# Performance work log

Hardware: AMD Instinct MI355X
Metric: run time of the kernel (lower is better)

## Reference

```python
import jax, jax.numpy as jnp
import numpy as np

H = 768      # hidden_size
NH = 12      # num_attention_heads
DH = H // NH # attention_head_size
FF = 3072    # intermediate_size
E = 4        # n_expert
B, S = 8, 512
EPS = 1e-12


def _layernorm(x, g, b):
    mu = jnp.mean(x, axis=-1, keepdims=True)
    var = jnp.var(x, axis=-1, keepdims=True)
    return (x - mu) * jax.lax.rsqrt(var + EPS) * g + b


def _expert_linear(x, W, b, expert_idx):
    # W: [E, in, out], b: [E, out]; gather per-sample expert weights, then batched GEMM.
    # Mathematically identical to running every expert then slicing (single_select_fwd).
    Wg = W[expert_idx]            # [B, in, out]
    bg = b[expert_idx]            # [B, out]
    return jnp.einsum('bsi,bio->bso', x, Wg) + bg[:, None, :]


def setup_inputs() -> dict:
    key = jax.random.key(0)
    ks = jax.random.split(key, 16)
    sc = 0.02
    inp = {
        'hidden_states': jax.random.normal(ks[0], (B, S, H), jnp.float32),
        'expert_idx': jax.random.randint(ks[1], (B,), 0, E, jnp.int64) if jax.config.read('jax_enable_x64') else jax.random.randint(ks[1], (B,), 0, E).astype(jnp.int32),
        'attention_mask': jnp.zeros((B, 1, 1, S), jnp.float32),
        'Wq': sc * jax.random.normal(ks[2], (E, H, H), jnp.float32),
        'bq': jnp.zeros((E, H), jnp.float32),
        'Wk': sc * jax.random.normal(ks[3], (E, H, H), jnp.float32),
        'bk': jnp.zeros((E, H), jnp.float32),
        'Wv': sc * jax.random.normal(ks[4], (E, H, H), jnp.float32),
        'bv': jnp.zeros((E, H), jnp.float32),
        'Wo': sc * jax.random.normal(ks[5], (E, H, H), jnp.float32),
        'bo': jnp.zeros((E, H), jnp.float32),
        'ln1_g': jnp.ones((H,), jnp.float32),
        'ln1_b': jnp.zeros((H,), jnp.float32),
        'Wi': sc * jax.random.normal(ks[6], (E, H, FF), jnp.float32),
        'bi': jnp.zeros((E, FF), jnp.float32),
        'Wout': sc * jax.random.normal(ks[7], (E, FF, H), jnp.float32),
        'bout': jnp.zeros((E, H), jnp.float32),
        'ln2_g': jnp.ones((H,), jnp.float32),
        'ln2_b': jnp.zeros((H,), jnp.float32),
    }
    return inp


def reference(hidden_states, expert_idx, attention_mask, Wq, bq, Wk, bk, Wv, bv,
              Wo, bo, ln1_g, ln1_b, Wi, bi, Wout, bout, ln2_g, ln2_b):
    b, s, h = hidden_states.shape
    # --- MoE self-attention (per-sample expert QKV) ---
    q = _expert_linear(hidden_states, Wq, bq, expert_idx).reshape(b, s, NH, DH).transpose(0, 2, 1, 3)
    k = _expert_linear(hidden_states, Wk, bk, expert_idx).reshape(b, s, NH, DH).transpose(0, 2, 1, 3)
    v = _expert_linear(hidden_states, Wv, bv, expert_idx).reshape(b, s, NH, DH).transpose(0, 2, 1, 3)
    scores = jnp.einsum('bhqd,bhkd->bhqk', q, k) / np.sqrt(DH).astype(np.float32)
    scores = scores + attention_mask
    probs = jax.nn.softmax(scores, axis=-1)
    ctx = jnp.einsum('bhqk,bhkd->bhqd', probs, v).transpose(0, 2, 1, 3).reshape(b, s, h)
    # --- MoE self-output: dense + residual + LN ---
    attn_out = _expert_linear(ctx, Wo, bo, expert_idx)
    x = _layernorm(attn_out + hidden_states, ln1_g, ln1_b)
    # --- MoE FFN: intermediate (GELU) + output + residual + LN ---
    hmid = jax.nn.gelu(_expert_linear(x, Wi, bi, expert_idx), approximate=False)
    ffn = _expert_linear(hmid, Wout, bout, expert_idx)
    return _layernorm(ffn + x, ln2_g, ln2_b)
```

## Files before the change

### kernel.cpp

```cpp
#include <hip/hip_runtime.h>
#include <cstdint>
#include <cstddef>

constexpr int CB  = 8;
constexpr int CS  = 512;
constexpr int CH  = 768;
constexpr int CNH = 12;
constexpr int CDH = 64;
constexpr int CFF = 3072;
constexpr int CE  = 4;
constexpr int C3H = 3 * CH;

using f32x4  = __attribute__((ext_vector_type(4))) float;
using bf16x8 = __attribute__((ext_vector_type(8))) short;

__device__ __forceinline__ short f2bf(float x) {
  union { float f; uint32_t u; } v; v.f = x;
  return (short)((v.u + 0x7fffu + ((v.u >> 16) & 1u)) >> 16);
}

__device__ __forceinline__ void gload_lds16(const void* g, void* l) {
  __builtin_amdgcn_global_load_lds((const __attribute__((address_space(1))) void*)g,
                                   (__attribute__((address_space(3))) void*)l,
                                   16, 0, 0);
}

#define VMCNT(n)  asm volatile("s_waitcnt vmcnt(" #n ")" ::: "memory")
#define SCHEDB()  __builtin_amdgcn_sched_barrier(0)

__global__ void cvt_bf16_kernel(const float* __restrict__ in, short* __restrict__ out, int n4) {
  int i = blockIdx.x * blockDim.x + threadIdx.x;
  if (i < n4) {
    float4 v = ((const float4*)in)[i];
    short4 o;
    o.x = f2bf(v.x); o.y = f2bf(v.y); o.z = f2bf(v.z); o.w = f2bf(v.w);
    ((short4*)out)[i] = o;
  }
}

__device__ __forceinline__ bool expert_used(const int* __restrict__ eidx, int e) {
  bool u = false;
#pragma unroll
  for (int s = 0; s < CB; ++s) u |= (eidx[s] == e);
  return u;
}

__device__ __forceinline__ void tpose_body(const float* __restrict__ Wb,
                                           short* __restrict__ Wtb, int K, int N) {
  __shared__ __align__(16) short Ts[64 * 68];
  const int n0 = blockIdx.x * 64, k0 = blockIdx.y * 64;
  const int t  = threadIdx.x;
  const int tn = t & 15, tk = t >> 4;
#pragma unroll
  for (int p = 0; p < 4; ++p) {
    int k = k0 + p * 16 + tk;
    float4 v = *(const float4*)(Wb + (size_t)k * N + n0 + tn * 4);
#pragma unroll
    for (int j = 0; j < 4; ++j)
      Ts[(tn * 4 + j) * 68 + p * 16 + tk] = f2bf(((const float*)&v)[j]);
  }
  __syncthreads();
#pragma unroll
  for (int p = 0; p < 4; ++p) {
    int n = n0 + p * 16 + tk;
    uint2 o = *(const uint2*)(Ts + (p * 16 + tk) * 68 + tn * 4);
    *(uint2*)(Wtb + (size_t)n * K + k0 + tn * 4) = o;
  }
}

__global__ void tpose_cvt_kernel(const float* __restrict__ W, short* __restrict__ Wt,
                                 const int* __restrict__ eidx, int K, int N) {
  const int e = blockIdx.z;
  if (!expert_used(eidx, e)) return;
  tpose_body(W + (size_t)e * K * N, Wt + (size_t)e * K * N, K, N);
}

__global__ void tpose4_kernel(const float* __restrict__ Wq, const float* __restrict__ Wk,
                              const float* __restrict__ Wv, const float* __restrict__ Wo,
                              const int* __restrict__ eidx,
                              short* __restrict__ Wqkvt, short* __restrict__ Wot) {
  const int z = blockIdx.z, e = z >> 2, m = z & 3;
  if (!expert_used(eidx, e)) return;
  const float* W = (m == 0) ? Wq : (m == 1) ? Wk : (m == 2) ? Wv : Wo;
  const float* Wb = W + (size_t)e * CH * CH;
  short* dst = (m == 3) ? (Wot + (size_t)e * CH * CH)
                        : (Wqkvt + ((size_t)e * C3H + m * CH) * CH);
  tpose_body(Wb, dst, CH, CH);
}

__global__ void qkv_bias_kernel(const float* __restrict__ bq, const float* __restrict__ bk,
                                const float* __restrict__ bv, float* __restrict__ dst) {
  int i = blockIdx.x * 256 + threadIdx.x;
  if (i >= CE * C3H) return;
  int e = i / C3H, r = i % C3H;
  int m = r / CH, c = r % CH;
  const float* s = (m == 0) ? bq : (m == 1) ? bk : bv;
  dst[i] = s[e * CH + c];
}

__device__ __forceinline__ void expert_sort(const int* __restrict__ eidx,
                                            uint32_t& epack, uint32_t& sortedPack) {
  int exv[CB];
#pragma unroll
  for (int s = 0; s < CB; ++s) exv[s] = eidx[s];
  epack = 0;
#pragma unroll
  for (int s = 0; s < CB; ++s) epack |= (uint32_t)exv[s] << (2 * s);
  int c0 = 0, c1 = 0, c2 = 0;
#pragma unroll
  for (int s = 0; s < CB; ++s) {
    c0 += (exv[s] == 0); c1 += (exv[s] == 1); c2 += (exv[s] == 2);
  }
  int p0 = 0, p1 = c0, p2 = c0 + c1, p3 = c0 + c1 + c2;
  sortedPack = 0;
#pragma unroll
  for (int s = 0; s < CB; ++s) {
    int ee = exv[s];
    int p = (ee == 0) ? p0 : (ee == 1) ? p1 : (ee == 2) ? p2 : p3;
    sortedPack |= (uint32_t)s << (4 * p);
    p0 += (ee == 0); p1 += (ee == 1); p2 += (ee == 2); p3 += (ee == 3);
  }
}

template <int BM, int NTN, int KSPLIT, int NJB, int NNB>
__device__ __forceinline__ void moe_decode(const int* __restrict__ eidx,
                                           int& e, int& mrow0, int& nt, int& ks) {
  constexpr int JC  = 4096 / BM;
  constexpr int MTS = CS / BM;
  constexpr int CHJ = JC / NJB;
  constexpr int CHN = NTN / NNB;
  constexpr int NKB = 8 / (NJB * NNB);
  constexpr int CHK = KSPLIT / NKB;
  uint32_t epack, sortedPack;
  expert_sort(eidx, epack, sortedPack);
  const int x = (int)blockIdx.x & 7;
  const int i = (int)blockIdx.x >> 3;
  const int kb = x / (NJB * NNB);
  const int rx = x - kb * (NJB * NNB);
  const int jb = rx / NNB, nb = rx - (rx / NNB) * NNB;
  const int nn = i % CHN;
  const int rem = i / CHN;
  const int jj = rem % CHJ;
  const int kk2 = rem / CHJ;
  const int j = jb * CHJ + jj;
  nt = nb * CHN + nn;
  ks = kb * CHK + kk2;
  const int sample = (int)((sortedPack >> (4 * (j / MTS))) & 7);
  e = (int)((epack >> (2 * sample)) & 3);
  mrow0 = sample * CS + (j % MTS) * BM;
}

template <int K, int NTN, int KSPLIT, int NJB, int NNB, int ACT, bool OB16>
__global__ __launch_bounds__(256, 2)
void gemm8_kernel(const short* __restrict__ A, const short* __restrict__ Wt,
                  const float* __restrict__ bias, const int* __restrict__ eidx,
                  char* __restrict__ out, char* __restrict__ out2,
                  size_t wtExpStride, int biasStride, int outLd, size_t outKsStride) {
  constexpr int BM = 128, BN = 192;
  constexpr int MI = 4, NI = 6;
  constexpr int NT = K / KSPLIT / 128;
  __shared__ __align__(16) short As[BM * 128];
  __shared__ __align__(16) short Bs[BN * 128];
  const int t = threadIdx.x, w = t >> 6, l = t & 63, lr = l & 15, lg = l >> 4;

  int e, mrow0, nt, ks;
  moe_decode<BM, NTN, KSPLIT, NJB, NNB>(eidx, e, mrow0, nt, ks);
  const int kBase = ks * NT * 128;

  const int srow = t >> 4;
  const int gcol = ((t & 15) ^ srow) * 8;
  const short* aSrc = A + (size_t)(mrow0 + srow) * K + kBase + gcol;
  const short* bSrc = Wt + (size_t)e * wtExpStride + (size_t)(nt * BN + srow) * K + kBase + gcol;
  const size_t iss16 = (size_t)16 * K;

  const int wrow = (w >> 1) * 64, wn = (w & 1) * 96;
  int aoff[4][MI], boff[4][NI];
#pragma unroll
  for (int kk = 0; kk < 4; ++kk) {
    const int c = (kk * 4 + lg) ^ lr;
#pragma unroll
    for (int mi = 0; mi < MI; ++mi)
      aoff[kk][mi] = (wrow + mi * 16 + lr) * 128 + c * 8;
#pragma unroll
    for (int ni = 0; ni < NI; ++ni)
      boff[kk][ni] = (wn + ni * 16 + lr) * 128 + c * 8;
  }

  f32x4 acc[MI][NI] = {};

  for (int kt = 0; kt < NT; ++kt) {
    {
      const short* as = aSrc + (size_t)kt * 128;
#pragma unroll
      for (int i = 0; i < 8; ++i)
        gload_lds16(as + i * iss16, &As[i * 2048 + t * 8]);
      const short* bs = bSrc + (size_t)kt * 128;
#pragma unroll
      for (int i = 0; i < 12; ++i)
        gload_lds16(bs + i * iss16, &Bs[i * 2048 + t * 8]);
    }
    VMCNT(0);
    __builtin_amdgcn_s_barrier();
    SCHEDB();
#pragma unroll
    for (int kk = 0; kk < 4; ++kk) {
      bf16x8 af[MI], bfr[NI];
#pragma unroll
      for (int ni = 0; ni < NI; ++ni) bfr[ni] = *(const bf16x8*)(&Bs[boff[kk][ni]]);
#pragma unroll
      for (int mi = 0; mi < MI; ++mi) af[mi] = *(const bf16x8*)(&As[aoff[kk][mi]]);
      __builtin_amdgcn_s_setprio(1);
#pragma unroll
      for (int mi = 0; mi < MI; ++mi)
#pragma unroll
        for (int ni = 0; ni < NI; ++ni)
          acc[mi][ni] = __builtin_amdgcn_mfma_f32_16x16x32_bf16(af[mi], bfr[ni],
                                                                acc[mi][ni], 0, 0, 0);
      __builtin_amdgcn_s_setprio(0);
    }
    __builtin_amdgcn_s_barrier();
    SCHEDB();
  }

  float* outF = (ks < 2) ? ((float*)out + (size_t)ks * outKsStride)
                         : ((float*)out2 + (size_t)(ks - 2) * outKsStride);
#pragma unroll
  for (int ni = 0; ni < NI; ++ni) {
    const int col = nt * BN + wn + ni * 16 + lr;
    const float bv = bias ? bias[e * biasStride + col] : 0.0f;
#pragma unroll
    for (int mi = 0; mi < MI; ++mi) {
      const int row0 = mrow0 + wrow + mi * 16 + lg * 4;
#pragma unroll
      for (int r = 0; r < 4; ++r) {
        float v = acc[mi][ni][r] + bv;
        if (ACT == 1) v = 0.5f * v * (1.0f + erff(v * 0.70710678118654752f));
        if (OB16) ((short*)out)[(size_t)(row0 + r) * outLd + col] = f2bf(v);
        else      outF[(size_t)(row0 + r) * outLd + col] = v;
      }
    }
  }
}

__global__ void attn_kernel(const short* __restrict__ QKV, const float* __restrict__ mask,
                            short* __restrict__ ctx) {
  __shared__ __align__(16) short Vt[2][64 * 40];
  __shared__ __align__(16) short Pt[4][2][16 * 40];
  const int bh = blockIdx.x;
  const int b = bh / CNH, h = bh % CNH;
  const int qt = blockIdx.y;
  const int t = threadIdx.x, w = t >> 6, l = t & 63, lr = l & 15, lg = l >> 4;

  const size_t bS = (size_t)b * CS;
  const short* Qh = QKV + bS * C3H + h * CDH;
  const short* Kh = Qh + CH;
  const short* Vh = Qh + 2 * CH;
  const float* mrow = mask + bS;

  const int qrow = qt * 64 + w * 16 + lr;
  bf16x8 qa[2];
  qa[0] = *(const bf16x8*)(Qh + (size_t)qrow * C3H + lg * 8);
  qa[1] = *(const bf16x8*)(Qh + (size_t)qrow * C3H + 32 + lg * 8);

  f32x4 o[4] = {};
  float lp[4] = {0.f, 0.f, 0.f, 0.f};

  const int dh = t & 63, kg = t >> 6;
  {
    short v8[8];
#pragma unroll
    for (int j = 0; j < 8; ++j) v8[j] = Vh[(size_t)(kg * 8 + j) * C3H + dh];
    uint32_t p0 = (uint32_t)(uint16_t)v8[0] | ((uint32_t)(uint16_t)v8[1] << 16);
    uint32_t p1 = (uint32_t)(uint16_t)v8[2] | ((uint32_t)(uint16_t)v8[3] << 16);
    uint32_t p2 = (uint32_t)(uint16_t)v8[4] | ((uint32_t)(uint16_t)v8[5] << 16);
    uint32_t p3 = (uint32_t)(uint16_t)v8[6] | ((uint32_t)(uint16_t)v8[7] << 16);
    uint4 pk = {p0, p1, p2, p3};
    *(uint4*)(&Vt[0][dh * 40 + kg * 8]) = pk;
  }

  for (int tt = 0; tt < CS / 32; ++tt) {
    const int k0 = tt * 32;
    __syncthreads();

    f32x4 sacc[2] = {};
#pragma unroll
    for (int n = 0; n < 2; ++n) {
      bf16x8 kb0 = *(const bf16x8*)(Kh + (size_t)(k0 + n * 16 + lr) * C3H + lg * 8);
      bf16x8 kb1 = *(const bf16x8*)(Kh + (size_t)(k0 + n * 16 + lr) * C3H + 32 + lg * 8);
      sacc[n] = __builtin_amdgcn_mfma_f32_16x16x32_bf16(qa[0], kb0, sacc[n], 0, 0, 0);
      sacc[n] = __builtin_amdgcn_mfma_f32_16x16x32_bf16(qa[1], kb1, sacc[n], 0, 0, 0);
    }

    if (tt + 1 < CS / 32) {
      const int k1 = k0 + 32;
      short v8[8];
#pragma unroll
      for (int j = 0; j < 8; ++j) v8[j] = Vh[(size_t)(k1 + kg * 8 + j) * C3H + dh];
      uint32_t p0 = (uint32_t)(uint16_t)v8[0] | ((uint32_t)(uint16_t)v8[1] << 16);
      uint32_t p1 = (uint32_t)(uint16_t)v8[2] | ((uint32_t)(uint16_t)v8[3] << 16);
      uint32_t p2 = (uint32_t)(uint16_t)v8[4] | ((uint32_t)(uint16_t)v8[5] << 16);
      uint32_t p3 = (uint32_t)(uint16_t)v8[6] | ((uint32_t)(uint16_t)v8[7] << 16);
      uint4 pk = {p0, p1, p2, p3};
      *(uint4*)(&Vt[(tt + 1) & 1][dh * 40 + kg * 8]) = pk;
    }

    const int pb = tt & 1;
#pragma unroll
    for (int n = 0; n < 2; ++n) {
      float mv = mrow[k0 + n * 16 + lr];
#pragma unroll
      for (int r = 0; r < 4; ++r) {
        float s = sacc[n][r] * 0.125f + mv;
        float e = __expf(s);
        lp[r] += e;
        Pt[w][pb][(lg * 4 + r) * 40 + n * 16 + lr] = f2bf(e);
      }
    }

    bf16x8 pa = *(const bf16x8*)(&Pt[w][pb][lr * 40 + lg * 8]);
#pragma unroll
    for (int d = 0; d < 4; ++d) {
      bf16x8 vbf = *(const bf16x8*)(&Vt[tt & 1][(d * 16 + lr) * 40 + lg * 8]);
      o[d] = __builtin_amdgcn_mfma_f32_16x16x32_bf16(pa, vbf, o[d], 0, 0, 0);
    }
  }

#pragma unroll
  for (int r = 0; r < 4; ++r) {
    float s = lp[r];
    s += __shfl_xor(s, 1); s += __shfl_xor(s, 2);
    s += __shfl_xor(s, 4); s += __shfl_xor(s, 8);
    lp[r] = 1.0f / s;
  }
#pragma unroll
  for (int d = 0; d < 4; ++d)
#pragma unroll
    for (int r = 0; r < 4; ++r) {
      int row = qt * 64 + w * 16 + lg * 4 + r;
      ctx[(bS + row) * CH + h * CDH + d * 16 + lr] = f2bf(o[d][r] * lp[r]);
    }
}

template <int NP>
__global__ void ln12_kernel(const float* __restrict__ p0, const float* __restrict__ p1,
                            const float* __restrict__ p2, const float* __restrict__ p3,
                            const float* __restrict__ res,
                            const float* __restrict__ btab, const int* __restrict__ eidx,
                            const float* __restrict__ g, const float* __restrict__ bta,
                            float* __restrict__ out32, short* __restrict__ out16) {
  const int row = blockIdx.x;
  const int l = threadIdx.x;
  const int e = eidx[row >> 9];
  const float* xr0 = p0 + (size_t)row * CH;
  const float* xr1 = p1 + (size_t)row * CH;
  const float* rr  = res + (size_t)row * CH;
  const float* bo  = btab + (size_t)e * CH;
  float4 v[3];
  float sum = 0.f, ss = 0.f;
#pragma unroll
  for (int j = 0; j < 3; ++j) {
    float4 a = *(const float4*)(xr0 + j * 256 + l * 4);
    float4 c = *(const float4*)(xr1 + j * 256 + l * 4);
    float4 b = *(const float4*)(rr + j * 256 + l * 4);
    float4 bb = *(const float4*)(bo + j * 256 + l * 4);
    a.x += c.x + b.x + bb.x; a.y += c.y + b.y + bb.y;
    a.z += c.z + b.z + bb.z; a.w += c.w + b.w + bb.w;
    if (NP >= 3) {
      float4 d2 = *(const float4*)(p2 + (size_t)row * CH + j * 256 + l * 4);
      a.x += d2.x; a.y += d2.y; a.z += d2.z; a.w += d2.w;
    }
    if (NP == 4) {
      float4 d3 = *(const float4*)(p3 + (size_t)row * CH + j * 256 + l * 4);
      a.x += d3.x; a.y += d3.y; a.z += d3.z; a.w += d3.w;
    }
    v[j] = a;
    sum += a.x + a.y + a.z + a.w;
    ss  += a.x * a.x + a.y * a.y + a.z * a.z + a.w * a.w;
  }
#pragma unroll
  for (int m = 1; m < 64; m <<= 1) { sum += __shfl_xor(sum, m); ss += __shfl_xor(ss, m); }
  const float mean = sum * (1.0f / CH);
  const float var  = ss * (1.0f / CH) - mean * mean;
  const float rstd = rsqrtf(var + 1e-12f);
#pragma unroll
  for (int j = 0; j < 3; ++j) {
    float4 gg = *(const float4*)(g   + j * 256 + l * 4);
    float4 bb = *(const float4*)(bta + j * 256 + l * 4);
    float4 a = v[j], y;
    y.x = (a.x - mean) * rstd * gg.x + bb.x;
    y.y = (a.y - mean) * rstd * gg.y + bb.y;
    y.z = (a.z - mean) * rstd * gg.z + bb.z;
    y.w = (a.w - mean) * rstd * gg.w + bb.w;
    *(float4*)(out32 + (size_t)row * CH + j * 256 + l * 4) = y;
    if (out16) {
      short4 o;
      o.x = f2bf(y.x); o.y = f2bf(y.y); o.z = f2bf(y.z); o.w = f2bf(y.w);
      *(short4*)(out16 + (size_t)row * CH + j * 256 + l * 4) = o;
    }
  }
}

extern "C" void kernel_launch(void* const* d_in, const int* in_sizes, int n_in,
                              void* d_out, int out_size, void* d_ws, size_t ws_size,
                              hipStream_t stream) {
  (void)in_sizes; (void)n_in; (void)out_size; (void)ws_size;
  const float* hidden = (const float*)d_in[0];
  const int*   eidx   = (const int*)d_in[1];
  const float* mask   = (const float*)d_in[2];
  const float* Wq   = (const float*)d_in[3];
  const float* bq   = (const float*)d_in[4];
  const float* Wk   = (const float*)d_in[5];
  const float* bk   = (const float*)d_in[6];
  const float* Wv   = (const float*)d_in[7];
  const float* bv   = (const float*)d_in[8];
  const float* Wo   = (const float*)d_in[9];
  const float* bo   = (const float*)d_in[10];
  const float* ln1g = (const float*)d_in[11];
  const float* ln1b = (const float*)d_in[12];
  const float* Wi   = (const float*)d_in[13];
  const float* bi   = (const float*)d_in[14];
  const float* Wout = (const float*)d_in[15];
  const float* bout = (const float*)d_in[16];
  const float* ln2g = (const float*)d_in[17];
  const float* ln2b = (const float*)d_in[18];

  char* ws = (char*)d_ws;
  size_t off = 0;
  auto alloc = [&](size_t bytes) {
    void* p = ws + off;
    off += (bytes + 255) & ~(size_t)255;
    return p;
  };
  const size_t M = (size_t)CB * CS;
  short* Xb    = (short*)alloc(M * CH * 2);
  char*  Rbig  = (char*)alloc(M * CFF * 2);
  char*  Rcx   = (char*)alloc(M * CH * 4);
  float* parts = (float*)alloc(2 * M * CH * 4);
  float* qkvbias = (float*)alloc(CE * C3H * 4);
  short* Wqkvt = (short*)alloc((size_t)CE * C3H * CH * 2);
  short* Wot   = (short*)alloc((size_t)CE * CH * CH * 2);
  short* Wit   = (short*)alloc((size_t)CE * CH * CFF * 2);
  short* Wo2t  = (short*)alloc((size_t)CE * CFF * CH * 2);
  short* QKVb = (short*)Rbig;
  short* hmid = (short*)Rbig;
  short* ctxb = (short*)Rcx;
  float* x1   = (float*)Rcx;
  short* x1b  = Xb;
  float* pp2  = (float*)Wqkvt;
  float* pp3  = pp2 + M * CH;

  const int n4 = (int)(M * CH / 4);
  cvt_bf16_kernel<<<(n4 + 255) / 256, 256, 0, stream>>>(hidden, Xb, n4);
  tpose4_kernel<<<dim3(CH / 64, CH / 64, 4 * CE), 256, 0, stream>>>(Wq, Wk, Wv, Wo, eidx, Wqkvt, Wot);
  tpose_cvt_kernel<<<dim3(CFF / 64, CH / 64, CE), 256, 0, stream>>>(Wi, Wit, eidx, CH, CFF);
  tpose_cvt_kernel<<<dim3(CH / 64, CFF / 64, CE), 256, 0, stream>>>(Wout, Wo2t, eidx, CFF, CH);
  qkv_bias_kernel<<<(CE * C3H + 255) / 256, 256, 0, stream>>>(bq, bk, bv, qkvbias);

  gemm8_kernel<CH, 12, 1, 4, 2, 0, true><<<384, 256, 0, stream>>>(
      Xb, Wqkvt, qkvbias, eidx, (char*)QKVb, nullptr, (size_t)C3H * CH, C3H, C3H, 0);
  attn_kernel<<<dim3(CB * CNH, CS / 64), 256, 0, stream>>>(QKVb, mask, ctxb);
  gemm8_kernel<CH, 4, 3, 4, 2, 0, false><<<384, 256, 0, stream>>>(
      ctxb, Wot, nullptr, eidx, (char*)parts, (char*)pp2, (size_t)CH * CH, CH, CH, M * CH);
  ln12_kernel<3><<<(int)M, 64, 0, stream>>>(parts, parts + M * CH, pp2, nullptr,
                                            hidden, bo, eidx, ln1g, ln1b, x1, x1b);
  gemm8_kernel<CH, 16, 1, 4, 2, 1, true><<<512, 256, 0, stream>>>(
      x1b, Wit, bi, eidx, (char*)hmid, nullptr, (size_t)CH * CFF, CFF, CFF, 0);
  gemm8_kernel<CFF, 4, 4, 2, 1, 0, false><<<512, 256, 0, stream>>>(
      hmid, Wo2t, nullptr, eidx, (char*)parts, (char*)pp2, (size_t)CFF * CH, CH, CH, M * CH);
  ln12_kernel<4><<<(int)M, 64, 0, stream>>>(parts, parts + M * CH, pp2, pp3,
                                            x1, bout, eidx, ln2g, ln2b, (float*)d_out, nullptr);
}
```

Before: 188.1 us.

## Add LDS-free direct-load GEMM for QKV and FFN-intermediate projections

Adds a new GEMM kernel in which each wave loads its A and B fragments straight from global memory into registers and issues MFMA, with no LDS staging and 64x64 tiles per wave. It replaces the LDS-tiled gemm8 kernel for the QKV projection and the GELU intermediate projection, using more blocks and a higher occupancy bound. The aim is to remove LDS traffic and barrier overhead and to improve occupancy. The cost is that blocks no longer share loads: each wave rereads the A rows from global memory or cache, with no double buffering or latency hiding beyond occupancy.

```diff
diff --git a/kernel.cpp b/kernel.cpp
--- a/kernel.cpp
+++ b/kernel.cpp
@@ -150,6 +150,69 @@
   mrow0 = sample * CS + (j % MTS) * BM;
 }
 
+template <int K, int NTG, int NJB, int NNB, int ACT, bool OB16>
+__global__ __launch_bounds__(256, 4)
+void gemmd_kernel(const short* __restrict__ A, const short* __restrict__ Wt,
+                  const float* __restrict__ bias, const int* __restrict__ eidx,
+                  char* __restrict__ out,
+                  size_t wtExpStride, int biasStride, int outLd) {
+  constexpr int JC = 64, MTS = 8;
+  constexpr int CHJ = JC / NJB, CHG = NTG / NNB;
+  const int t = threadIdx.x, w = t >> 6, l = t & 63, lr = l & 15, lg = l >> 4;
+
+  uint32_t epack, sortedPack;
+  expert_sort(eidx, epack, sortedPack);
+  const int x = (int)blockIdx.x & 7;
+  const int i = (int)blockIdx.x >> 3;
+  const int jb = x / NNB, nb = x % NNB;
+  const int gg = i % CHG, jj = i / CHG;
+  const int j = jb * CHJ + jj;
+  const int ntile = (nb * CHG + gg) * 4 + w;
+  const int sample = (int)((sortedPack >> (4 * (j / MTS))) & 7);
+  const int e = (int)((epack >> (2 * sample)) & 3);
+  const int mrow0 = sample * CS + (j % MTS) * 64;
+
+  const short* Ab = A + (size_t)mrow0 * K;
+  const short* Bb = Wt + (size_t)e * wtExpStride + (size_t)(ntile * 64) * K;
+  const int laneoff = lr * K + lg * 8;
+
+  f32x4 acc[4][4] = {};
+
+  for (int kt = 0; kt < K / 32; ++kt) {
+    const int ko = kt * 32 + laneoff;
+    bf16x8 af[4], bfr[4];
+#pragma unroll
+    for (int mi = 0; mi < 4; ++mi)
+      af[mi] = *(const bf16x8*)(Ab + (size_t)mi * 16 * K + ko);
+#pragma unroll
+    for (int ni = 0; ni < 4; ++ni)
+      bfr[ni] = *(const bf16x8*)(Bb + (size_t)ni * 16 * K + ko);
+#pragma unroll
+    for (int mi = 0; mi < 4; ++mi)
+#pragma unroll
+      for (int ni = 0; ni < 4; ++ni)
+        acc[mi][ni] = __builtin_amdgcn_mfma_f32_16x16x32_bf16(af[mi], bfr[ni],
+                                                              acc[mi][ni], 0, 0, 0);
+  }
+
+#pragma unroll
+  for (int ni = 0; ni < 4; ++ni) {
+    const int col = ntile * 64 + ni * 16 + lr;
+    const float bv = bias ? bias[e * biasStride + col] : 0.0f;
+#pragma unroll
+    for (int mi = 0; mi < 4; ++mi) {
+      const int row0 = mrow0 + mi * 16 + lg * 4;
+#pragma unroll
+      for (int r = 0; r < 4; ++r) {
+        float v = acc[mi][ni][r] + bv;
+        if (ACT == 1) v = 0.5f * v * (1.0f + erff(v * 0.70710678118654752f));
+        if (OB16) ((short*)out)[(size_t)(row0 + r) * outLd + col] = f2bf(v);
+        else      ((float*)out)[(size_t)(row0 + r) * outLd + col] = v;
+      }
+    }
+  }
+}
+
 template <int K, int NTN, int KSPLIT, int NJB, int NNB, int ACT, bool OB16>
 __global__ __launch_bounds__(256, 2)
 void gemm8_kernel(const short* __restrict__ A, const short* __restrict__ Wt,
@@ -456,15 +519,15 @@
   tpose_cvt_kernel<<<dim3(CH / 64, CFF / 64, CE), 256, 0, stream>>>(Wout, Wo2t, eidx, CFF, CH);
   qkv_bias_kernel<<<(CE * C3H + 255) / 256, 256, 0, stream>>>(bq, bk, bv, qkvbias);
 
-  gemm8_kernel<CH, 12, 1, 4, 2, 0, true><<<384, 256, 0, stream>>>(
-      Xb, Wqkvt, qkvbias, eidx, (char*)QKVb, nullptr, (size_t)C3H * CH, C3H, C3H, 0);
+  gemmd_kernel<CH, 9, 8, 1, 0, true><<<576, 256, 0, stream>>>(
+      Xb, Wqkvt, qkvbias, eidx, (char*)QKVb, (size_t)C3H * CH, C3H, C3H);
   attn_kernel<<<dim3(CB * CNH, CS / 64), 256, 0, stream>>>(QKVb, mask, ctxb);
   gemm8_kernel<CH, 4, 3, 4, 2, 0, false><<<384, 256, 0, stream>>>(
       ctxb, Wot, nullptr, eidx, (char*)parts, (char*)pp2, (size_t)CH * CH, CH, CH, M * CH);
   ln12_kernel<3><<<(int)M, 64, 0, stream>>>(parts, parts + M * CH, pp2, nullptr,
                                             hidden, bo, eidx, ln1g, ln1b, x1, x1b);
-  gemm8_kernel<CH, 16, 1, 4, 2, 1, true><<<512, 256, 0, stream>>>(
-      x1b, Wit, bi, eidx, (char*)hmid, nullptr, (size_t)CH * CFF, CFF, CFF, 0);
+  gemmd_kernel<CH, 12, 4, 2, 1, true><<<768, 256, 0, stream>>>(
+      x1b, Wit, bi, eidx, (char*)hmid, (size_t)CH * CFF, CFF, CFF);
   gemm8_kernel<CFF, 4, 4, 2, 1, 0, false><<<512, 256, 0, stream>>>(
       hmid, Wo2t, nullptr, eidx, (char*)parts, (char*)pp2, (size_t)CFF * CH, CH, CH, M * CH);
   ln12_kernel<4><<<(int)M, 64, 0, stream>>>(parts, parts + M * CH, pp2, pp3,
```

After: 283.0 us. 1.5x slower.
